# Optimization experiments

Measured on AMD Instinct MI355X. Metric: run time of the kernel, lower is better.

The kernel has to match this reference:

```python
import jax, jax.numpy as jnp
import numpy as np

DIM = 1024
N_HEADS = 16
HEAD_DIM = DIM // N_HEADS
HIDDEN = 2816
SEQ = 4096
BATCH = 1
NORM_EPS = 1e-5


def setup_inputs() -> dict:
    key = jax.random.key(0)
    ks = jax.random.split(key, 9)
    s = 1.0 / np.sqrt(DIM)
    return {
        "x": jax.random.normal(ks[0], (BATCH, SEQ, DIM), jnp.float32),
        "wq": jax.random.normal(ks[1], (DIM, DIM), jnp.float32) * s,
        "wk": jax.random.normal(ks[2], (DIM, DIM), jnp.float32) * s,
        "wv": jax.random.normal(ks[3], (DIM, DIM), jnp.float32) * s,
        "wo": jax.random.normal(ks[4], (DIM, DIM), jnp.float32) * s,
        "w1": jax.random.normal(ks[5], (DIM, HIDDEN), jnp.float32) * s,
        "w2": jax.random.normal(ks[6], (HIDDEN, DIM), jnp.float32) / np.sqrt(HIDDEN),
        "w3": jax.random.normal(ks[7], (DIM, HIDDEN), jnp.float32) * s,
        "g_attn_norm": jnp.ones((DIM,), jnp.float32),
        "g_ffn_norm": jnp.ones((DIM,), jnp.float32),
    }


def rmsnorm(x, g):
    # x: [b, s, d]; compute in fp32 as in the torch module, then cast back
    xf = x.astype(jnp.float32)
    n = xf * jax.lax.rsqrt(jnp.mean(xf * xf, axis=-1, keepdims=True) + NORM_EPS)
    return n.astype(x.dtype) * g


def attention(x, wq, wk, wv, wo):
    b, s, _ = x.shape
    q = (x @ wq).reshape(b, s, N_HEADS, HEAD_DIM).transpose(0, 2, 1, 3)  # [b,h,s,hd]
    k = (x @ wk).reshape(b, s, N_HEADS, HEAD_DIM).transpose(0, 2, 1, 3)
    v = (x @ wv).reshape(b, s, N_HEADS, HEAD_DIM).transpose(0, 2, 1, 3)
    scores = jnp.einsum("bhqd,bhkd->bhqk", q, k) / np.sqrt(HEAD_DIM)
    causal = jnp.tril(jnp.ones((s, s), bool))
    scores = jnp.where(causal, scores, -jnp.inf)
    probs = jax.nn.softmax(scores.astype(jnp.float32), axis=-1).astype(q.dtype)
    out = jnp.einsum("bhqk,bhkd->bhqd", probs, v)
    out = out.transpose(0, 2, 1, 3).reshape(b, s, DIM)
    return out @ wo


def feed_forward(x, w1, w2, w3):
    return (jax.nn.silu(x @ w1) * (x @ w3)) @ w2


def reference(x, wq, wk, wv, wo, w1, w2, w3, g_attn_norm, g_ffn_norm):
    h = x + attention(rmsnorm(x, g_attn_norm), wq, wk, wv, wo)
    out = h + feed_forward(rmsnorm(h, g_ffn_norm), w1, w2, w3)
    return out
```

## Files before the change

### kernel.cpp

```cpp
#include <hip/hip_runtime.h>
#include <stdint.h>


typedef unsigned short u16;
typedef unsigned int u32;
typedef __attribute__((ext_vector_type(8))) short short8;
typedef __attribute__((ext_vector_type(4))) float f32x4;

#define GLD16(G, L) __builtin_amdgcn_global_load_lds( \
    (__attribute__((address_space(1))) void*)(G),      \
    (__attribute__((address_space(3))) void*)(L), 16, 0, 0)

__device__ __forceinline__ u16 f2bf(float f) {
  u32 u = __builtin_bit_cast(u32, f);
  u32 r = u + 0x7fffu + ((u >> 16) & 1u);
  return (u16)(r >> 16);
}
__device__ __forceinline__ float bf2f(u16 b) {
  u32 u = (u32)b << 16;
  return __builtin_bit_cast(float, u);
}
__device__ __forceinline__ u32 pk_bf16(float lo, float hi) {
  u32 r;
  asm("v_cvt_pk_bf16_f32 %0, %1, %2" : "=v"(r) : "v"(lo), "v"(hi));
  return r;
}

__global__ __launch_bounds__(256) void k_tc4(const float* __restrict__ s0,
                                             const float* __restrict__ s1,
                                             const float* __restrict__ s2,
                                             const float* __restrict__ s3,
                                             u16* __restrict__ out, int R, int C) {
  const int z = blockIdx.z;
  const float* in = (z == 0) ? s0 : (z == 1) ? s1 : (z == 2) ? s2 : s3;
  u16* o = out + (size_t)z * R * C;
  __shared__ float t[32][33];
  const int tx = threadIdx.x & 31, ty = threadIdx.x >> 5;
  const int c0 = blockIdx.x * 32, r0 = blockIdx.y * 32;
#pragma unroll
  for (int i = 0; i < 32; i += 8)
    t[ty + i][tx] = in[(size_t)(r0 + ty + i) * C + (c0 + tx)];
  __syncthreads();
#pragma unroll
  for (int i = 0; i < 32; i += 8)
    o[(size_t)(c0 + ty + i) * R + (r0 + tx)] = f2bf(t[tx][ty + i]);
}

__global__ __launch_bounds__(256) void k_rms(const float* __restrict__ x,
                                             const float* __restrict__ g,
                                             u16* __restrict__ o) {
  const int row = blockIdx.x, tid = threadIdx.x;
  const float4 v = ((const float4*)(x + (size_t)row * 1024))[tid];
  float ss = v.x * v.x + v.y * v.y + v.z * v.z + v.w * v.w;
#pragma unroll
  for (int ofs = 32; ofs > 0; ofs >>= 1) ss += __shfl_xor(ss, ofs);
  __shared__ float red[4];
  if ((tid & 63) == 0) red[tid >> 6] = ss;
  __syncthreads();
  const float s = rsqrtf((red[0] + red[1] + red[2] + red[3]) * (1.f / 1024.f) + 1e-5f);
  const float4 gv = ((const float4*)g)[tid];
  u32 lo = (u32)f2bf(v.x * s * gv.x) | ((u32)f2bf(v.y * s * gv.y) << 16);
  u32 hi = (u32)f2bf(v.z * s * gv.z) | ((u32)f2bf(v.w * s * gv.w) << 16);
  *(uint2*)(o + (size_t)row * 1024 + tid * 4) = make_uint2(lo, hi);
}

template <int EPI, int TN>
__global__ __launch_bounds__(256) void k_gemm(const u16* __restrict__ A,
                                              const u16* __restrict__ Bt,
                                              u16* __restrict__ Obf,
                                              float* __restrict__ Of,
                                              const float* __restrict__ Rz,
                                              int M, int N, int K) {
  constexpr int NFR = TN / 32;
  __shared__ __align__(16) u16 As[128 * 32];
  __shared__ __align__(16) u16 Bs[TN * 32];
  const int tid = threadIdx.x;
  const int lane = tid & 63, wave = tid >> 6;
  const int wr = wave >> 1, wc = wave & 1;
  const int li = lane & 15, lg = lane >> 4;
  const int row0 = blockIdx.y * 128, col0 = blockIdx.x * TN;

  f32x4 acc[4][NFR] = {};
  const int sr = tid >> 2, sc = (tid & 3) * 8;
  const u16* ag = A + (size_t)(row0 + sr) * K + sc;
  const u16* bg = Bt + (size_t)(col0 + sr) * K + sc;
  u16* al = As + tid * 8;
  u16* bl = Bs + tid * 8;
  const size_t rstep = (size_t)64 * K;

  for (int k0 = 0; k0 < K; k0 += 32) {
    __syncthreads();
    GLD16(ag + k0, al);
    GLD16(ag + rstep + k0, al + 2048);
    GLD16(bg + k0, bl);
    if constexpr (TN == 128) GLD16(bg + rstep + k0, bl + 2048);
    __syncthreads();
    short8 af[4], bfr[NFR];
#pragma unroll
    for (int m = 0; m < 4; ++m)
      af[m] = *(const short8*)(As + (wr * 64 + m * 16 + li) * 32 + lg * 8);
#pragma unroll
    for (int n = 0; n < NFR; ++n)
      bfr[n] = *(const short8*)(Bs + (wc * (TN / 2) + n * 16 + li) * 32 + lg * 8);
#pragma unroll
    for (int m = 0; m < 4; ++m)
#pragma unroll
      for (int n = 0; n < NFR; ++n)
        acc[m][n] = __builtin_amdgcn_mfma_f32_16x16x32_bf16(af[m], bfr[n], acc[m][n], 0, 0, 0);
  }

#pragma unroll
  for (int m = 0; m < 4; ++m) {
    const int row = row0 + wr * 64 + m * 16 + lg * 4;
#pragma unroll
    for (int n = 0; n < NFR; ++n) {
      const int col = col0 + wc * (TN / 2) + n * 16 + li;
#pragma unroll
      for (int r = 0; r < 4; ++r) {
        const size_t idx = (size_t)(row + r) * N + col;
        if (EPI == 0) Obf[idx] = f2bf(acc[m][n][r]);
        else          Of[idx] = acc[m][n][r] + Rz[idx];
      }
    }
  }
}

__global__ __launch_bounds__(256) void k_ffn13(const u16* __restrict__ A,
                                               const u16* __restrict__ B1,
                                               const u16* __restrict__ B3,
                                               u16* __restrict__ O,
                                               int M, int N, int K) {
  __shared__ __align__(16) u16 As[128 * 32];
  __shared__ __align__(16) u16 B1s[64 * 32];
  __shared__ __align__(16) u16 B3s[64 * 32];
  const int tid = threadIdx.x;
  const int lane = tid & 63, wave = tid >> 6;
  const int wr = wave >> 1, wc = wave & 1;
  const int li = lane & 15, lg = lane >> 4;
  const int row0 = blockIdx.y * 128, col0 = blockIdx.x * 64;

  f32x4 a1[4][2] = {}, a3[4][2] = {};
  const int sr = tid >> 2, sc = (tid & 3) * 8;
  const u16* ag = A + (size_t)(row0 + sr) * K + sc;
  const u16* b1g = B1 + (size_t)(col0 + sr) * K + sc;
  const u16* b3g = B3 + (size_t)(col0 + sr) * K + sc;
  u16* al = As + tid * 8;
  u16* b1l = B1s + tid * 8;
  u16* b3l = B3s + tid * 8;
  const size_t rstep = (size_t)64 * K;

  for (int k0 = 0; k0 < K; k0 += 32) {
    __syncthreads();
    GLD16(ag + k0, al);
    GLD16(ag + rstep + k0, al + 2048);
    GLD16(b1g + k0, b1l);
    GLD16(b3g + k0, b3l);
    __syncthreads();
    short8 af[4], b1f[2], b3f[2];
#pragma unroll
    for (int m = 0; m < 4; ++m)
      af[m] = *(const short8*)(As + (wr * 64 + m * 16 + li) * 32 + lg * 8);
#pragma unroll
    for (int n = 0; n < 2; ++n) {
      b1f[n] = *(const short8*)(B1s + (wc * 32 + n * 16 + li) * 32 + lg * 8);
      b3f[n] = *(const short8*)(B3s + (wc * 32 + n * 16 + li) * 32 + lg * 8);
    }
#pragma unroll
    for (int m = 0; m < 4; ++m)
#pragma unroll
      for (int n = 0; n < 2; ++n) {
        a1[m][n] = __builtin_amdgcn_mfma_f32_16x16x32_bf16(af[m], b1f[n], a1[m][n], 0, 0, 0);
        a3[m][n] = __builtin_amdgcn_mfma_f32_16x16x32_bf16(af[m], b3f[n], a3[m][n], 0, 0, 0);
      }
  }

#pragma unroll
  for (int m = 0; m < 4; ++m) {
    const int row = row0 + wr * 64 + m * 16 + lg * 4;
#pragma unroll
    for (int n = 0; n < 2; ++n) {
      const int col = col0 + wc * 32 + n * 16 + li;
#pragma unroll
      for (int r = 0; r < 4; ++r) {
        const float g1 = a1[m][n][r], g3 = a3[m][n][r];
        const float sl = g1 / (1.f + __expf(-g1));
        O[(size_t)(row + r) * N + col] = f2bf(sl * g3);
      }
    }
  }
}

__global__ __launch_bounds__(512) void k_attn(const u16* __restrict__ qkv,
                                              u16* __restrict__ o) {
  const int LD = 3072;
  const int h = blockIdx.x & 15;
  const int qb = 31 - (blockIdx.x >> 4);
  const int q0 = qb * 128;
  const int tid = threadIdx.x, lane = tid & 63, w = tid >> 6;
  const int li = lane & 15, lg = lane >> 4;
  const int swzB = (li & 7) << 4;

  __shared__ __align__(16) u16 Ks[64 * 64];
  __shared__ __align__(16) u16 Vt[64 * 64];
  __shared__ __align__(16) u16 Ps[8 * 16 * 64];

  const int qrow = q0 + w * 16 + li;
  const u16* qp = qkv + (size_t)qrow * LD + h * 64;
  const float QS = 0.125f * 1.44269504f;
  short8 qf0, qf1;
#pragma unroll
  for (int j = 0; j < 8; ++j) {
    qf0[j] = (short)f2bf(bf2f(qp[lg * 8 + j]) * QS);
    qf1[j] = (short)f2bf(bf2f(qp[32 + lg * 8 + j]) * QS);
  }

  const int krow = tid >> 3;
  const u16* kg = qkv + 1024 + h * 64 + ((tid & 7) ^ (krow & 7)) * 8;
  u16* klds = Ks + tid * 8;

  const int vd0 = (tid & 31) * 2;
  const int vkq = tid >> 5;
  const u16* vg = qkv + 2048 + h * 64 + vd0;
  u16* vl0 = Vt + (size_t)vd0 * 64 + (((vkq * 8) ^ ((vd0 & 7) << 4)) >> 1);
  u16* vl1 = Vt + (size_t)(vd0 + 1) * 64 + (((vkq * 8) ^ (((vd0 + 1) & 7) << 4)) >> 1);

  u16* pw = Ps + w * 1024 + li * 64;

  float msm = -1e30f, lsm = 0.f;
  f32x4 accO[4] = {};
  u32 vld[4];

  {
#pragma unroll
    for (int i = 0; i < 4; ++i) vld[i] = *(const u32*)(vg + (size_t)(vkq * 4 + i) * LD);
  }

  const int kend = q0 + 64;
  const int wqmax = q0 + w * 16 + 15;
  for (int k0 = 0; k0 <= kend; k0 += 64) {
    __syncthreads();
    GLD16(kg + (size_t)(k0 + krow) * LD, klds);
    {
      u32 lo0 = (vld[0] & 0xffffu) | (vld[1] << 16);
      u32 lo1 = (vld[2] & 0xffffu) | (vld[3] << 16);
      u32 hi0 = (vld[0] >> 16) | (vld[1] & 0xffff0000u);
      u32 hi1 = (vld[2] >> 16) | (vld[3] & 0xffff0000u);
      *(uint2*)vl0 = make_uint2(lo0, lo1);
      *(uint2*)vl1 = make_uint2(hi0, hi1);
    }
    __syncthreads();
    if (k0 + 64 <= kend) {
      const u16* vp = vg + (size_t)(k0 + 64) * LD;
#pragma unroll
      for (int i = 0; i < 4; ++i) vld[i] = *(const u32*)(vp + (size_t)(vkq * 4 + i) * LD);
    }

    if (k0 <= wqmax) {
      f32x4 st[4];
#pragma unroll
      for (int f = 0; f < 4; ++f) {
        const u16* kp = Ks + (size_t)(f * 16 + li) * 64;
        const short8 ka0 = *(const short8*)(kp + (((lg * 16) ^ swzB) >> 1));
        const short8 ka1 = *(const short8*)(kp + (((64 + lg * 16) ^ swzB) >> 1));
        f32x4 z = {};
        z = __builtin_amdgcn_mfma_f32_16x16x32_bf16(ka0, qf0, z, 0, 0, 0);
        st[f] = __builtin_amdgcn_mfma_f32_16x16x32_bf16(ka1, qf1, z, 0, 0, 0);
      }

      float sv[16];
      float mloc = -1e30f;
      if (k0 + 63 <= q0 + w * 16) {
#pragma unroll
        for (int f = 0; f < 4; ++f)
#pragma unroll
          for (int r = 0; r < 4; ++r) {
            sv[f * 4 + r] = st[f][r];
            mloc = fmaxf(mloc, sv[f * 4 + r]);
          }
      } else {
#pragma unroll
        for (int f = 0; f < 4; ++f)
#pragma unroll
          for (int r = 0; r < 4; ++r) {
            const int kg2 = k0 + f * 16 + lg * 4 + r;
            sv[f * 4 + r] = (kg2 > qrow) ? -1e30f : st[f][r];
            mloc = fmaxf(mloc, sv[f * 4 + r]);
          }
      }
      mloc = fmaxf(mloc, __shfl_xor(mloc, 16));
      mloc = fmaxf(mloc, __shfl_xor(mloc, 32));
      if (!__all(mloc - msm <= 8.0f)) {
        const float mnew = fmaxf(msm, mloc);
        const float alpha = __builtin_amdgcn_exp2f(msm - mnew);
        lsm *= alpha;
#pragma unroll
        for (int n = 0; n < 4; ++n) {
          accO[n][0] *= alpha; accO[n][1] *= alpha;
          accO[n][2] *= alpha; accO[n][3] *= alpha;
        }
        msm = mnew;
      }
      float psum = 0.f;
#pragma unroll
      for (int f = 0; f < 4; ++f) {
        const float p0 = __builtin_amdgcn_exp2f(sv[f * 4 + 0] - msm);
        const float p1 = __builtin_amdgcn_exp2f(sv[f * 4 + 1] - msm);
        const float p2 = __builtin_amdgcn_exp2f(sv[f * 4 + 2] - msm);
        const float p3 = __builtin_amdgcn_exp2f(sv[f * 4 + 3] - msm);
        psum += (p0 + p1) + (p2 + p3);
        *(uint2*)(pw + (((f * 32 + lg * 8) ^ swzB) >> 1)) =
            make_uint2(pk_bf16(p0, p1), pk_bf16(p2, p3));
      }
      psum += __shfl_xor(psum, 16);
      psum += __shfl_xor(psum, 32);
      lsm += psum;

#pragma unroll
      for (int kk = 0; kk < 2; ++kk) {
        const int cofs = ((kk * 64 + lg * 16) ^ swzB) >> 1;
        const short8 pf = *(const short8*)(pw + cofs);
#pragma unroll
        for (int n = 0; n < 4; ++n) {
          const short8 vf = *(const short8*)(Vt + (size_t)(n * 16 + li) * 64 + cofs);
          accO[n] = __builtin_amdgcn_mfma_f32_16x16x32_bf16(vf, pf, accO[n], 0, 0, 0);
        }
      }
    }
  }

  const float linv = 1.f / lsm;
  u16* op = o + (size_t)qrow * 1024 + h * 64;
#pragma unroll
  for (int n = 0; n < 4; ++n) {
    *(uint2*)(op + n * 16 + lg * 4) =
        make_uint2(pk_bf16(accO[n][0] * linv, accO[n][1] * linv),
                   pk_bf16(accO[n][2] * linv, accO[n][3] * linv));
  }
}

extern "C" void kernel_launch(void* const* d_in, const int* in_sizes, int n_in,
                              void* d_out, int out_size, void* d_ws, size_t ws_size,
                              hipStream_t stream) {
  const float* x  = (const float*)d_in[0];
  const float* wq = (const float*)d_in[1];
  const float* wk = (const float*)d_in[2];
  const float* wv = (const float*)d_in[3];
  const float* wo = (const float*)d_in[4];
  const float* w1 = (const float*)d_in[5];
  const float* w2 = (const float*)d_in[6];
  const float* w3 = (const float*)d_in[7];
  const float* ga = (const float*)d_in[8];
  const float* gf = (const float*)d_in[9];
  float* out = (float*)d_out;

  char* p = (char*)d_ws;
  auto take = [&](size_t n) { char* r = p; p += (n + 255) & ~(size_t)255; return r; };
  u16* wqkvo_t = (u16*)take(4ull * 1024 * 1024 * 2);
  u16* w13_t   = (u16*)take(2ull * 2816 * 1024 * 2);
  u16* w2_t    = (u16*)take(1024ull * 2816 * 2);
  u16* xn      = (u16*)take(4096ull * 1024 * 2);
  u16* qkvb    = (u16*)take(4096ull * 3072 * 2);
  u16* atn     = (u16*)take(4096ull * 1024 * 2);
  float* hb    = (float*)take(4096ull * 1024 * 4);
  u16* hn      = (u16*)take(4096ull * 1024 * 2);
  u16* ffb     = (u16*)take(4096ull * 2816 * 2);

  u16* wqkv_t = wqkvo_t;
  u16* wo_t   = wqkvo_t + 3ull * 1024 * 1024;
  u16* w1_t   = w13_t;
  u16* w3_t   = w13_t + 2816ull * 1024;

  k_tc4<<<dim3(32, 32, 4), 256, 0, stream>>>(wq, wk, wv, wo, wqkvo_t, 1024, 1024);
  k_tc4<<<dim3(88, 32, 2), 256, 0, stream>>>(w1, w3, w1, w3, w13_t, 1024, 2816);
  k_tc4<<<dim3(32, 88, 1), 256, 0, stream>>>(w2, w2, w2, w2, w2_t, 2816, 1024);

  k_rms<<<4096, 256, 0, stream>>>(x, ga, xn);
  k_gemm<0, 128><<<dim3(24, 32), 256, 0, stream>>>(xn, wqkv_t, qkvb, nullptr, nullptr, 4096, 3072, 1024);
  k_attn<<<512, 512, 0, stream>>>(qkvb, atn);
  k_gemm<1, 64><<<dim3(16, 32), 256, 0, stream>>>(atn, wo_t, nullptr, hb, x, 4096, 1024, 1024);
  k_rms<<<4096, 256, 0, stream>>>(hb, gf, hn);
  k_ffn13<<<dim3(44, 32), 256, 0, stream>>>(hn, w1_t, w3_t, ffb, 4096, 2816, 1024);
  k_gemm<1, 64><<<dim3(16, 32), 256, 0, stream>>>(ffb, w2_t, nullptr, out, hb, 4096, 1024, 2816);
}
```

Measured before the change: 311.4 us.

## Split attention KV range across blocks with paired q-tiles and a merge kernel

The attention kernel now splits each query tile's KV range into two halves, processed by different blocks. Each block handles a pair of query tiles (p and 31-p) so work per block is balanced under the causal mask. Blocks write unnormalized fp32 partial outputs plus max and sum stats, and a new merge kernel combines them into bf16 output. The goal is to remove the load imbalance of causal attention, at the cost of extra fp32 partial traffic, one more launch, and workspace aliasing with later buffers.

```diff
diff --git a/kernel.cpp b/kernel.cpp
--- a/kernel.cpp
+++ b/kernel.cpp
@@ -191,28 +191,21 @@
 }
 
 __global__ __launch_bounds__(512) void k_attn(const u16* __restrict__ qkv,
-                                              u16* __restrict__ o) {
+                                              float* __restrict__ Opart,
+                                              float* __restrict__ ml) {
   const int LD = 3072;
-  const int h = blockIdx.x & 15;
-  const int qb = 31 - (blockIdx.x >> 4);
-  const int q0 = qb * 128;
+  const int b = blockIdx.x;
+  const int h = b & 15;
+  const int p = (b >> 4) >> 1;
+  const int j = (b >> 4) & 1;
   const int tid = threadIdx.x, lane = tid & 63, w = tid >> 6;
   const int li = lane & 15, lg = lane >> 4;
   const int swzB = (li & 7) << 4;
+  const float QS = 0.125f * 1.44269504f;
 
   __shared__ __align__(16) u16 Ks[64 * 64];
   __shared__ __align__(16) u16 Vt[64 * 64];
   __shared__ __align__(16) u16 Ps[8 * 16 * 64];
-
-  const int qrow = q0 + w * 16 + li;
-  const u16* qp = qkv + (size_t)qrow * LD + h * 64;
-  const float QS = 0.125f * 1.44269504f;
-  short8 qf0, qf1;
-#pragma unroll
-  for (int j = 0; j < 8; ++j) {
-    qf0[j] = (short)f2bf(bf2f(qp[lg * 8 + j]) * QS);
-    qf1[j] = (short)f2bf(bf2f(qp[32 + lg * 8 + j]) * QS);
-  }
 
   const int krow = tid >> 3;
   const u16* kg = qkv + 1024 + h * 64 + ((tid & 7) ^ (krow & 7)) * 8;
@@ -223,118 +216,160 @@
   const u16* vg = qkv + 2048 + h * 64 + vd0;
   u16* vl0 = Vt + (size_t)vd0 * 64 + (((vkq * 8) ^ ((vd0 & 7) << 4)) >> 1);
   u16* vl1 = Vt + (size_t)(vd0 + 1) * 64 + (((vkq * 8) ^ (((vd0 + 1) & 7) << 4)) >> 1);
-
   u16* pw = Ps + w * 1024 + li * 64;
 
-  float msm = -1e30f, lsm = 0.f;
-  f32x4 accO[4] = {};
-  u32 vld[4];
-
-  {
-#pragma unroll
-    for (int i = 0; i < 4; ++i) vld[i] = *(const u32*)(vg + (size_t)(vkq * 4 + i) * LD);
-  }
-
-  const int kend = q0 + 64;
-  const int wqmax = q0 + w * 16 + 15;
-  for (int k0 = 0; k0 <= kend; k0 += 64) {
-    __syncthreads();
-    GLD16(kg + (size_t)(k0 + krow) * LD, klds);
-    {
-      u32 lo0 = (vld[0] & 0xffffu) | (vld[1] << 16);
-      u32 lo1 = (vld[2] & 0xffffu) | (vld[3] << 16);
-      u32 hi0 = (vld[0] >> 16) | (vld[1] & 0xffff0000u);
-      u32 hi1 = (vld[2] >> 16) | (vld[3] & 0xffff0000u);
-      *(uint2*)vl0 = make_uint2(lo0, lo1);
-      *(uint2*)vl1 = make_uint2(hi0, hi1);
-    }
-    __syncthreads();
-    if (k0 + 64 <= kend) {
-      const u16* vp = vg + (size_t)(k0 + 64) * LD;
-#pragma unroll
-      for (int i = 0; i < 4; ++i) vld[i] = *(const u32*)(vp + (size_t)(vkq * 4 + i) * LD);
-    }
-
-    if (k0 <= wqmax) {
-      f32x4 st[4];
-#pragma unroll
-      for (int f = 0; f < 4; ++f) {
-        const u16* kp = Ks + (size_t)(f * 16 + li) * 64;
-        const short8 ka0 = *(const short8*)(kp + (((lg * 16) ^ swzB) >> 1));
-        const short8 ka1 = *(const short8*)(kp + (((64 + lg * 16) ^ swzB) >> 1));
-        f32x4 z = {};
-        z = __builtin_amdgcn_mfma_f32_16x16x32_bf16(ka0, qf0, z, 0, 0, 0);
-        st[f] = __builtin_amdgcn_mfma_f32_16x16x32_bf16(ka1, qf1, z, 0, 0, 0);
-      }
-
-      float sv[16];
-      float mloc = -1e30f;
-      if (k0 + 63 <= q0 + w * 16) {
-#pragma unroll
-        for (int f = 0; f < 4; ++f)
-#pragma unroll
-          for (int r = 0; r < 4; ++r) {
-            sv[f * 4 + r] = st[f][r];
-            mloc = fmaxf(mloc, sv[f * 4 + r]);
+  for (int sub = 0; sub < 2; ++sub) {
+    const int qb = sub ? (31 - p) : p;
+    const int q0 = qb * 128;
+    const int t0 = j ? (qb + 1) : 0;
+    const int t1 = j ? (2 * qb + 2) : (qb + 1);
+    const int qrow = q0 + w * 16 + li;
+    const int wqmax = q0 + w * 16 + 15;
+
+    const u16* qp = qkv + (size_t)qrow * LD + h * 64;
+    short8 qf0, qf1;
+#pragma unroll
+    for (int jj = 0; jj < 8; ++jj) {
+      qf0[jj] = (short)f2bf(bf2f(qp[lg * 8 + jj]) * QS);
+      qf1[jj] = (short)f2bf(bf2f(qp[32 + lg * 8 + jj]) * QS);
+    }
+
+    float msm = -1e30f, lsm = 0.f;
+    f32x4 accO[4] = {};
+    u32 vld[4];
+#pragma unroll
+    for (int i = 0; i < 4; ++i)
+      vld[i] = *(const u32*)(vg + (size_t)(t0 * 64 + vkq * 4 + i) * LD);
+
+    for (int t = t0; t < t1; ++t) {
+      const int k0 = t * 64;
+      __syncthreads();
+      GLD16(kg + (size_t)(k0 + krow) * LD, klds);
+      {
+        u32 lo0 = (vld[0] & 0xffffu) | (vld[1] << 16);
+        u32 lo1 = (vld[2] & 0xffffu) | (vld[3] << 16);
+        u32 hi0 = (vld[0] >> 16) | (vld[1] & 0xffff0000u);
+        u32 hi1 = (vld[2] >> 16) | (vld[3] & 0xffff0000u);
+        *(uint2*)vl0 = make_uint2(lo0, lo1);
+        *(uint2*)vl1 = make_uint2(hi0, hi1);
+      }
+      __syncthreads();
+      if (t + 1 < t1) {
+        const u16* vp = vg + (size_t)(t + 1) * 64 * LD;
+#pragma unroll
+        for (int i = 0; i < 4; ++i) vld[i] = *(const u32*)(vp + (size_t)(vkq * 4 + i) * LD);
+      }
+
+      if (k0 <= wqmax) {
+        f32x4 st[4];
+#pragma unroll
+        for (int f = 0; f < 4; ++f) {
+          const u16* kp = Ks + (size_t)(f * 16 + li) * 64;
+          const short8 ka0 = *(const short8*)(kp + (((lg * 16) ^ swzB) >> 1));
+          const short8 ka1 = *(const short8*)(kp + (((64 + lg * 16) ^ swzB) >> 1));
+          f32x4 z = {};
+          z = __builtin_amdgcn_mfma_f32_16x16x32_bf16(ka0, qf0, z, 0, 0, 0);
+          st[f] = __builtin_amdgcn_mfma_f32_16x16x32_bf16(ka1, qf1, z, 0, 0, 0);
+        }
+
+        float sv[16];
+        float mloc = -1e30f;
+        if (k0 + 63 <= q0 + w * 16) {
+#pragma unroll
+          for (int f = 0; f < 4; ++f)
+#pragma unroll
+            for (int r = 0; r < 4; ++r) {
+              sv[f * 4 + r] = st[f][r];
+              mloc = fmaxf(mloc, sv[f * 4 + r]);
+            }
+        } else {
+#pragma unroll
+          for (int f = 0; f < 4; ++f)
+#pragma unroll
+            for (int r = 0; r < 4; ++r) {
+              const int kg2 = k0 + f * 16 + lg * 4 + r;
+              sv[f * 4 + r] = (kg2 > qrow) ? -1e30f : st[f][r];
+              mloc = fmaxf(mloc, sv[f * 4 + r]);
+            }
+        }
+        mloc = fmaxf(mloc, __shfl_xor(mloc, 16));
+        mloc = fmaxf(mloc, __shfl_xor(mloc, 32));
+        if (!__all(mloc - msm <= 8.0f)) {
+          const float mnew = fmaxf(msm, mloc);
+          const float alpha = __builtin_amdgcn_exp2f(msm - mnew);
+          lsm *= alpha;
+#pragma unroll
+          for (int n = 0; n < 4; ++n) {
+            accO[n][0] *= alpha; accO[n][1] *= alpha;
+            accO[n][2] *= alpha; accO[n][3] *= alpha;
           }
-      } else {
-#pragma unroll
-        for (int f = 0; f < 4; ++f)
-#pragma unroll
-          for (int r = 0; r < 4; ++r) {
-            const int kg2 = k0 + f * 16 + lg * 4 + r;
-            sv[f * 4 + r] = (kg2 > qrow) ? -1e30f : st[f][r];
-            mloc = fmaxf(mloc, sv[f * 4 + r]);
+          msm = mnew;
+        }
+        float psum = 0.f;
+#pragma unroll
+        for (int f = 0; f < 4; ++f) {
+          const float p0 = __builtin_amdgcn_exp2f(sv[f * 4 + 0] - msm);
+          const float p1 = __builtin_amdgcn_exp2f(sv[f * 4 + 1] - msm);
+          const float p2 = __builtin_amdgcn_exp2f(sv[f * 4 + 2] - msm);
+          const float p3 = __builtin_amdgcn_exp2f(sv[f * 4 + 3] - msm);
+          psum += (p0 + p1) + (p2 + p3);
+          *(uint2*)(pw + (((f * 32 + lg * 8) ^ swzB) >> 1)) =
+              make_uint2(pk_bf16(p0, p1), pk_bf16(p2, p3));
+        }
+        psum += __shfl_xor(psum, 16);
+        psum += __shfl_xor(psum, 32);
+        lsm += psum;
+
+#pragma unroll
+        for (int kk = 0; kk < 2; ++kk) {
+          const int cofs = ((kk * 64 + lg * 16) ^ swzB) >> 1;
+          const short8 pf = *(const short8*)(pw + cofs);
+#pragma unroll
+          for (int n = 0; n < 4; ++n) {
+            const short8 vf = *(const short8*)(Vt + (size_t)(n * 16 + li) * 64 + cofs);
+            accO[n] = __builtin_amdgcn_mfma_f32_16x16x32_bf16(vf, pf, accO[n], 0, 0, 0);
           }
-      }
-      mloc = fmaxf(mloc, __shfl_xor(mloc, 16));
-      mloc = fmaxf(mloc, __shfl_xor(mloc, 32));
-      if (!__all(mloc - msm <= 8.0f)) {
-        const float mnew = fmaxf(msm, mloc);
-        const float alpha = __builtin_amdgcn_exp2f(msm - mnew);
-        lsm *= alpha;
-#pragma unroll
-        for (int n = 0; n < 4; ++n) {
-          accO[n][0] *= alpha; accO[n][1] *= alpha;
-          accO[n][2] *= alpha; accO[n][3] *= alpha;
         }
-        msm = mnew;
-      }
-      float psum = 0.f;
-#pragma unroll
-      for (int f = 0; f < 4; ++f) {
-        const float p0 = __builtin_amdgcn_exp2f(sv[f * 4 + 0] - msm);
-        const float p1 = __builtin_amdgcn_exp2f(sv[f * 4 + 1] - msm);
-        const float p2 = __builtin_amdgcn_exp2f(sv[f * 4 + 2] - msm);
-        const float p3 = __builtin_amdgcn_exp2f(sv[f * 4 + 3] - msm);
-        psum += (p0 + p1) + (p2 + p3);
-        *(uint2*)(pw + (((f * 32 + lg * 8) ^ swzB) >> 1)) =
-            make_uint2(pk_bf16(p0, p1), pk_bf16(p2, p3));
-      }
-      psum += __shfl_xor(psum, 16);
-      psum += __shfl_xor(psum, 32);
-      lsm += psum;
-
-#pragma unroll
-      for (int kk = 0; kk < 2; ++kk) {
-        const int cofs = ((kk * 64 + lg * 16) ^ swzB) >> 1;
-        const short8 pf = *(const short8*)(pw + cofs);
-#pragma unroll
-        for (int n = 0; n < 4; ++n) {
-          const short8 vf = *(const short8*)(Vt + (size_t)(n * 16 + li) * 64 + cofs);
-          accO[n] = __builtin_amdgcn_mfma_f32_16x16x32_bf16(vf, pf, accO[n], 0, 0, 0);
-        }
-      }
-    }
-  }
-
-  const float linv = 1.f / lsm;
-  u16* op = o + (size_t)qrow * 1024 + h * 64;
-#pragma unroll
-  for (int n = 0; n < 4; ++n) {
-    *(uint2*)(op + n * 16 + lg * 4) =
-        make_uint2(pk_bf16(accO[n][0] * linv, accO[n][1] * linv),
-                   pk_bf16(accO[n][2] * linv, accO[n][3] * linv));
+      }
+    }
+
+    const int item = (h * 32 + qb) * 2 + j;
+    float* op = Opart + (size_t)item * 8192 + (w * 16 + li) * 64 + lg * 4;
+#pragma unroll
+    for (int n = 0; n < 4; ++n)
+      *(f32x4*)(op + n * 16) = accO[n];
+    if (lg == 0) {
+      ml[item * 256 + w * 16 + li] = msm;
+      ml[item * 256 + 128 + w * 16 + li] = lsm;
+    }
+  }
+}
+
+__global__ __launch_bounds__(256) void k_amerge(const float* __restrict__ Opart,
+                                                const float* __restrict__ ml,
+                                                u16* __restrict__ o) {
+  const int b = blockIdx.x;
+  const int h = b & 15, qb = b >> 4;
+  const int q = threadIdx.x >> 1;
+  const int dh = (threadIdx.x & 1) * 32;
+  const int i0 = (h * 32 + qb) * 2;
+  const float m0 = ml[i0 * 256 + q], l0 = ml[i0 * 256 + 128 + q];
+  const float m1 = ml[(i0 + 1) * 256 + q], l1 = ml[(i0 + 1) * 256 + 128 + q];
+  const float M = fmaxf(m0, m1);
+  const float s0 = __builtin_amdgcn_exp2f(m0 - M);
+  const float s1 = __builtin_amdgcn_exp2f(m1 - M);
+  const float L = s0 * l0 + s1 * l1;
+  const float r0 = s0 / L, r1 = s1 / L;
+  const float* p0 = Opart + (size_t)i0 * 8192 + q * 64 + dh;
+  const float* p1 = p0 + 8192;
+  u16* op = o + (size_t)(qb * 128 + q) * 1024 + h * 64 + dh;
+#pragma unroll
+  for (int dd = 0; dd < 32; dd += 4) {
+    const f32x4 a = *(const f32x4*)(p0 + dd);
+    const f32x4 c = *(const f32x4*)(p1 + dd);
+    *(uint2*)(op + dd) =
+        make_uint2(pk_bf16(a[0] * r0 + c[0] * r1, a[1] * r0 + c[1] * r1),
+                   pk_bf16(a[2] * r0 + c[2] * r1, a[3] * r0 + c[3] * r1));
   }
 }
 
@@ -361,9 +396,12 @@
   u16* xn      = (u16*)take(4096ull * 1024 * 2);
   u16* qkvb    = (u16*)take(4096ull * 3072 * 2);
   u16* atn     = (u16*)take(4096ull * 1024 * 2);
-  float* hb    = (float*)take(4096ull * 1024 * 4);
-  u16* hn      = (u16*)take(4096ull * 1024 * 2);
-  u16* ffb     = (u16*)take(4096ull * 2816 * 2);
+  char* uni    = take(48234496);
+  float* Opart = (float*)uni;
+  float* mlb   = (float*)(uni + 1024ull * 8192 * 4);
+  float* hb    = (float*)uni;
+  u16* hn      = (u16*)(uni + 4096ull * 1024 * 4);
+  u16* ffb     = (u16*)(uni + 4096ull * 1024 * 6);
 
   u16* wqkv_t = wqkvo_t;
   u16* wo_t   = wqkvo_t + 3ull * 1024 * 1024;
@@ -376,7 +414,8 @@
 
   k_rms<<<4096, 256, 0, stream>>>(x, ga, xn);
   k_gemm<0, 128><<<dim3(24, 32), 256, 0, stream>>>(xn, wqkv_t, qkvb, nullptr, nullptr, 4096, 3072, 1024);
-  k_attn<<<512, 512, 0, stream>>>(qkvb, atn);
+  k_attn<<<512, 512, 0, stream>>>(qkvb, Opart, mlb);
+  k_amerge<<<512, 256, 0, stream>>>(Opart, mlb, atn);
   k_gemm<1, 64><<<dim3(16, 32), 256, 0, stream>>>(atn, wo_t, nullptr, hb, x, 4096, 1024, 1024);
   k_rms<<<4096, 256, 0, stream>>>(hb, gf, hn);
   k_ffn13<<<dim3(44, 32), 256, 0, stream>>>(hn, w1_t, w3_t, ffb, 4096, 2816, 1024);
```

New measurement: 297.7 us. 1.05x faster.
